# Optimization experiments

Measured on AMD Instinct MI355X. Metric: run time of the kernel, lower is better.

The kernel has to match this reference:

```python
import jax, jax.numpy as jnp
import numpy as np
import math

NBINS = 10
POOL = 8


def setup_inputs() -> dict:
    key = jax.random.key(0)
    x = jax.random.normal(key, (32, 1, 512, 512), dtype=jnp.float32)
    return {"x": x}


def _hog(x):
    # Sobel kernels: (out=2, in=1, 3, 3); channel 0 = horizontal, channel 1 = vertical.
    sob = jnp.array([[1., 0., -1.], [2., 0., -2.], [1., 0., -1.]], dtype=x.dtype)
    w = jnp.stack([sob, sob.T])[:, None, :, :]
    gxy = jax.lax.conv_general_dilated(
        x, w, window_strides=(1, 1), padding=((1, 1), (1, 1)),
        rhs_dilation=(1, 1), dimension_numbers=("NCHW", "OIHW", "NCHW"))
    gx, gy = gxy[:, 0], gxy[:, 1]            # (n, h, w)
    mag = jnp.sqrt(gx * gx + gy * gy)        # gxy.norm(dim=1)
    phase = jnp.arctan2(gx, gy)
    phase_int = phase / math.pi * NBINS
    # torch: out.scatter_(1, floor(phase_int).long() % nbins, mag) on a zero tensor.
    # NOTE: the subsequent out.scatter_add(...) in the source is OUT-OF-PLACE and its
    # result is discarded, so only the floor-bin scatter contributes. Reproduced faithfully.
    bins = jnp.mod(jnp.floor(phase_int).astype(jnp.int32), NBINS)  # (n, h, w), in [0, nbins)
    onehot = bins[:, None, :, :] == jnp.arange(NBINS, dtype=jnp.int32)[None, :, None, None]
    out = jnp.where(onehot, mag[:, None, :, :], jnp.zeros((), dtype=x.dtype))  # (n, nbins, h, w)
    # AvgPool2d(pool=8, stride=8, padding=0): h, w divisible by POOL.
    n, nb, h, wd = out.shape
    pooled = out.reshape(n, nb, h // POOL, POOL, wd // POOL, POOL).mean(axis=(3, 5))
    return pooled


def reference(x):
    # Original forward runs under torch.no_grad(); mirror with stop_gradient.
    return _hog(jax.lax.stop_gradient(x))
```

## Files before the change

### kernel.cpp

```cpp
#include <hip/hip_runtime.h>


namespace {
constexpr int H = 512, W = 512, NB = 10;
}

typedef __attribute__((ext_vector_type(2))) float f32x2;

__device__ __forceinline__ f32x2 vfma2(f32x2 a, f32x2 b, f32x2 c) {
#if __has_builtin(__builtin_elementwise_fma)
    return __builtin_elementwise_fma(a, b, c);
#else
    f32x2 r; r.x = fmaf(a.x, b.x, c.x); r.y = fmaf(a.y, b.y, c.y); return r;
#endif
}

__device__ __forceinline__ void load_row(const float* __restrict__ img,
                                         int ry, int x0, bool lok, bool rok,
                                         float (&R)[10]) {
    if (ry >= 0 && ry < H) {
        const float* p = img + (size_t)ry * W + x0;
        R[0] = lok ? p[-1] : 0.0f;
        const float4 a = *reinterpret_cast<const float4*>(p);
        const float4 b = *reinterpret_cast<const float4*>(p + 4);
        R[1] = a.x; R[2] = a.y; R[3] = a.z; R[4] = a.w;
        R[5] = b.x; R[6] = b.y; R[7] = b.z; R[8] = b.w;
        R[9] = rok ? p[8] : 0.0f;
    } else {
#pragma unroll
        for (int i = 0; i < 10; ++i) R[i] = 0.0f;
    }
}

__global__ __launch_bounds__(256) void hog_kernel(const float* __restrict__ xin,
                                                  float* __restrict__ out) {
    const int tid  = threadIdx.x;
    const int wid  = (blockIdx.x << 2) + (tid >> 6);
    const int lane = tid & 63;

    const int c  = lane >> 1;
    const int h  = lane & 1;

    const int cg  = (wid << 5) + c;
    const int n   = cg >> 12;
    const int rem = cg & 4095;
    const int ph  = rem >> 6;
    const int pw  = rem & 63;

    const int x0 = pw * 8;
    const int yb = ph * 8 + h * 4;

    const float* img = xin + (size_t)n * H * W;
    const bool lok = (pw > 0), rok = (pw < 63);

    const float PI32 = 3.14159274101257324f;
    const float C10  = __fmul_rn(__fdiv_rn(1.0f, PI32), 10.0f);

    const float P0 =  3.1826723f, P1 = -1.0513758f, P2 = 0.5734066f,
                P3 = -0.2709868f, P4 =  0.0663202f;
    const float EPSW = 1.25e-4f;

    f32x2 acc2[5];
#pragma unroll
    for (int p = 0; p < 5; ++p) acc2[p] = (f32x2){0.0f, 0.0f};

    auto deposit = [&](int b, float v) {
        const bool  hi = b >= 5;
        const int   q5 = hi ? (b - 5) : b;
        const f32x2 P  = hi ? (f32x2){0.0f, v} : (f32x2){v, 0.0f};
#pragma unroll
        for (int p = 0; p < 5; ++p) {
            const float g = (q5 == p) ? 1.0f : 0.0f;
            acc2[p] = vfma2(P, (f32x2){g, g}, acc2[p]);
        }
    };

    auto process_row = [&](const float (&T)[10], const float (&M)[10],
                           const float (&B)[10]) {
#pragma unroll
        for (int j = 0; j < 8; ++j) {
            const float t0 = T[j], t1 = T[j + 1], t2 = T[j + 2];
            const float m0 = M[j],                 m2 = M[j + 2];
            const float b0 = B[j], b1 = B[j + 1], b2 = B[j + 2];

            const float gx = ((((t0 - t2) + 2.0f * m0) - 2.0f * m2) + b0) - b2;
            const float gy = ((((t0 + 2.0f * t1) + t2) - b0) - 2.0f * b1) - b2;

            const float mag = __builtin_amdgcn_sqrtf(gx * gx + gy * gy);

            const float ax  = fabsf(gx);
            const float ay  = __uint_as_float(__float_as_uint(gy) ^
                                              (__float_as_uint(gx) & 0x80000000u));
            const float aay = fabsf(ay);

            const bool  q   = ax > aay;
            const float den = q ? ax : aay;
            const float num = q ? ay : ax;
            const float t   = num * __builtin_amdgcn_rcpf(den);
            const float u   = t * t;
            float p = fmaf(P4, u, P3);
            p = fmaf(p, u, P2);
            p = fmaf(p, u, P1);
            p = fmaf(p, u, P0);
            const float s = t * p;
            const float w = q ? (5.0f - s) : ((ay > 0.0f) ? s : (10.0f - s));

            const float dist = fabsf(w - rintf(w));
            const bool flagged = !(dist >= EPSW);

            int   bi;
            float dep;
            if (!flagged) {
                bi  = (int)w;
                dep = mag;
            } else {
                const float phs = atan2f(gx, gy);
                const float w10 = __fmul_rn(phs, C10);
                bi = (int)floorf(w10);
                bi %= 10;
                if (bi < 0) bi += 10;
                float half = 0.0f;
                const float rk  = rintf(w10);
                const float eps = fmaxf(4.0f * fabsf(w10) * 1.1920929e-7f, 1.5e-6f);
                if (fabsf(w10 - rk) < eps && mag < 4.6f) {
                    const int k  = (int)rk;
                    int kb = k % 10;       if (kb < 0) kb += 10;
                    int ka = (k - 1) % 10; if (ka < 0) ka += 10;
                    const int balt = (bi == kb) ? ka : kb;
                    half = 0.5f * mag;
                    deposit(balt, half);
                }
                dep = mag - half;
            }

            deposit(bi, dep);
        }
    };

    float R0[10], R1[10], R2[10], R3[10], R4[10], R5[10];
    load_row(img, yb - 1, x0, lok, rok, R0);
    load_row(img, yb,     x0, lok, rok, R1);
    load_row(img, yb + 1, x0, lok, rok, R2);
    load_row(img, yb + 2, x0, lok, rok, R3);
    process_row(R0, R1, R2);
    load_row(img, yb + 3, x0, lok, rok, R4);
    process_row(R1, R2, R3);
    load_row(img, yb + 4, x0, lok, rok, R5);
    process_row(R2, R3, R4);
    process_row(R3, R4, R5);

    float v0 = 0.0f, v1 = 0.0f, v2 = 0.0f, v3 = 0.0f, v4 = 0.0f;
#pragma unroll
    for (int p = 0; p < 5; ++p) {
        const float sx = acc2[p].x + __shfl_xor(acc2[p].x, 1, 64);
        const float sy = acc2[p].y + __shfl_xor(acc2[p].y, 1, 64);
        const float vq = h ? sy : sx;
        v0 = (p == 0) ? vq : v0;
        v1 = (p == 1) ? vq : v1;
        v2 = (p == 2) ? vq : v2;
        v3 = (p == 3) ? vq : v3;
        v4 = (p == 4) ? vq : v4;
    }

    const float inv = 1.0f / 64.0f;
    const size_t obase = (((size_t)n * NB) * 64 + (size_t)ph) * 64 + (size_t)pw
                       + (size_t)h * 5 * 4096;
    out[obase]            = v0 * inv;
    out[obase + 1 * 4096] = v1 * inv;
    out[obase + 2 * 4096] = v2 * inv;
    out[obase + 3 * 4096] = v3 * inv;
    out[obase + 4 * 4096] = v4 * inv;
}

extern "C" void kernel_launch(void* const* d_in, const int* in_sizes, int n_in,
                              void* d_out, int out_size, void* d_ws, size_t ws_size,
                              hipStream_t stream) {
    const float* x = (const float*)d_in[0];
    float* out = (float*)d_out;
    hipLaunchKernelGGL(hog_kernel, dim3(1024), dim3(256), 0, stream, x, out);
}
```

Baseline: 21.07 us.

## Split each pooling cell across four lanes and share Sobel partial sums

Each 8x8 cell is now handled by four lanes of two rows each instead of two lanes of four rows, doubling the grid to 2048 blocks. Per-row vertical sums and differences are precomputed so gx and gy each need only a few ops, with the exact-order Sobel recomputed only on the rare flagged path for bitwise-faithful tie handling. The costs are more redundant halo row loads (4 rows per 2 output rows), an extra shuffle stage, and half the lanes idle during stores.

```diff
diff --git a/kernel.cpp b/kernel.cpp
--- a/kernel.cpp
+++ b/kernel.cpp
@@ -38,17 +38,17 @@
     const int wid  = (blockIdx.x << 2) + (tid >> 6);
     const int lane = tid & 63;
 
-    const int c  = lane >> 1;
-    const int h  = lane & 1;
+    const int c   = lane >> 2;
+    const int sub = lane & 3;
 
-    const int cg  = (wid << 5) + c;
+    const int cg  = (wid << 4) + c;
     const int n   = cg >> 12;
     const int rem = cg & 4095;
     const int ph  = rem >> 6;
     const int pw  = rem & 63;
 
     const int x0 = pw * 8;
-    const int yb = ph * 8 + h * 4;
+    const int yb = ph * 8 + sub * 2;
 
     const float* img = xin + (size_t)n * H * W;
     const bool lok = (pw > 0), rok = (pw < 63);
@@ -77,14 +77,16 @@
 
     auto process_row = [&](const float (&T)[10], const float (&M)[10],
                            const float (&B)[10]) {
+        float S[10], D[10];
+#pragma unroll
+        for (int i = 0; i < 10; ++i) {
+            S[i] = fmaf(2.0f, M[i], T[i]) + B[i];
+            D[i] = T[i] - B[i];
+        }
 #pragma unroll
         for (int j = 0; j < 8; ++j) {
-            const float t0 = T[j], t1 = T[j + 1], t2 = T[j + 2];
-            const float m0 = M[j],                 m2 = M[j + 2];
-            const float b0 = B[j], b1 = B[j + 1], b2 = B[j + 2];
-
-            const float gx = ((((t0 - t2) + 2.0f * m0) - 2.0f * m2) + b0) - b2;
-            const float gy = ((((t0 + 2.0f * t1) + t2) - b0) - 2.0f * b1) - b2;
+            const float gx = S[j] - S[j + 2];
+            const float gy = fmaf(2.0f, D[j + 1], D[j] + D[j + 2]);
 
             const float mag = __builtin_amdgcn_sqrtf(gx * gx + gy * gy);
 
@@ -114,7 +116,14 @@
                 bi  = (int)w;
                 dep = mag;
             } else {
-                const float phs = atan2f(gx, gy);
+                const float t0 = T[j], t1 = T[j + 1], t2 = T[j + 2];
+                const float m0 = M[j],                 m2 = M[j + 2];
+                const float b0 = B[j], b1 = B[j + 1], b2 = B[j + 2];
+                const float gxs = ((((t0 - t2) + 2.0f * m0) - 2.0f * m2) + b0) - b2;
+                const float gys = ((((t0 + 2.0f * t1) + t2) - b0) - 2.0f * b1) - b2;
+                const float mgs = __builtin_amdgcn_sqrtf(gxs * gxs + gys * gys);
+
+                const float phs = atan2f(gxs, gys);
                 const float w10 = __fmul_rn(phs, C10);
                 bi = (int)floorf(w10);
                 bi %= 10;
@@ -122,39 +131,38 @@
                 float half = 0.0f;
                 const float rk  = rintf(w10);
                 const float eps = fmaxf(4.0f * fabsf(w10) * 1.1920929e-7f, 1.5e-6f);
-                if (fabsf(w10 - rk) < eps && mag < 4.6f) {
+                if (fabsf(w10 - rk) < eps && mgs < 4.6f) {
                     const int k  = (int)rk;
                     int kb = k % 10;       if (kb < 0) kb += 10;
                     int ka = (k - 1) % 10; if (ka < 0) ka += 10;
                     const int balt = (bi == kb) ? ka : kb;
-                    half = 0.5f * mag;
+                    half = 0.5f * mgs;
                     deposit(balt, half);
                 }
-                dep = mag - half;
+                dep = mgs - half;
             }
 
             deposit(bi, dep);
         }
     };
 
-    float R0[10], R1[10], R2[10], R3[10], R4[10], R5[10];
+    float R0[10], R1[10], R2[10], R3[10];
     load_row(img, yb - 1, x0, lok, rok, R0);
     load_row(img, yb,     x0, lok, rok, R1);
     load_row(img, yb + 1, x0, lok, rok, R2);
     load_row(img, yb + 2, x0, lok, rok, R3);
     process_row(R0, R1, R2);
-    load_row(img, yb + 3, x0, lok, rok, R4);
     process_row(R1, R2, R3);
-    load_row(img, yb + 4, x0, lok, rok, R5);
-    process_row(R2, R3, R4);
-    process_row(R3, R4, R5);
 
     float v0 = 0.0f, v1 = 0.0f, v2 = 0.0f, v3 = 0.0f, v4 = 0.0f;
 #pragma unroll
     for (int p = 0; p < 5; ++p) {
-        const float sx = acc2[p].x + __shfl_xor(acc2[p].x, 1, 64);
-        const float sy = acc2[p].y + __shfl_xor(acc2[p].y, 1, 64);
-        const float vq = h ? sy : sx;
+        float sx = acc2[p].x, sy = acc2[p].y;
+        sx += __shfl_xor(sx, 1, 64);
+        sx += __shfl_xor(sx, 2, 64);
+        sy += __shfl_xor(sy, 1, 64);
+        sy += __shfl_xor(sy, 2, 64);
+        const float vq = (sub & 1) ? sy : sx;
         v0 = (p == 0) ? vq : v0;
         v1 = (p == 1) ? vq : v1;
         v2 = (p == 2) ? vq : v2;
@@ -162,14 +170,16 @@
         v4 = (p == 4) ? vq : v4;
     }
 
-    const float inv = 1.0f / 64.0f;
-    const size_t obase = (((size_t)n * NB) * 64 + (size_t)ph) * 64 + (size_t)pw
-                       + (size_t)h * 5 * 4096;
-    out[obase]            = v0 * inv;
-    out[obase + 1 * 4096] = v1 * inv;
-    out[obase + 2 * 4096] = v2 * inv;
-    out[obase + 3 * 4096] = v3 * inv;
-    out[obase + 4 * 4096] = v4 * inv;
+    if (sub < 2) {
+        const float inv = 1.0f / 64.0f;
+        const size_t obase = (((size_t)n * NB) * 64 + (size_t)ph) * 64 + (size_t)pw
+                           + (size_t)sub * 5 * 4096;
+        out[obase]            = v0 * inv;
+        out[obase + 1 * 4096] = v1 * inv;
+        out[obase + 2 * 4096] = v2 * inv;
+        out[obase + 3 * 4096] = v3 * inv;
+        out[obase + 4 * 4096] = v4 * inv;
+    }
 }
 
 extern "C" void kernel_launch(void* const* d_in, const int* in_sizes, int n_in,
@@ -177,5 +187,5 @@
                               hipStream_t stream) {
     const float* x = (const float*)d_in[0];
     float* out = (float*)d_out;
-    hipLaunchKernelGGL(hog_kernel, dim3(1024), dim3(256), 0, stream, x, out);
+    hipLaunchKernelGGL(hog_kernel, dim3(2048), dim3(256), 0, stream, x, out);
 }
```

Result: no change. 21.10 us (+0.1%).
